# Optimization experiments

Measured on AMD Instinct MI355X. Metric: run time of the kernel, lower is better.

Reference implementation:

```python
import jax, jax.numpy as jnp
import numpy as np

N_EXPERTS = 64
TOPK = 4
DIM = 2048
B_T = 8192


def setup_inputs() -> dict:
    key = jax.random.key(0)
    k1, k2 = jax.random.split(key)
    x = jax.random.normal(k1, (B_T, DIM), jnp.float32)
    W = jax.random.normal(k2, (N_EXPERTS, DIM), jnp.float32) * 0.02  # nn.Linear weight (out, in)
    router_bias = jnp.zeros((N_EXPERTS,), jnp.float32)  # registered buffer, init zeros
    return {"x": x, "W": W, "router_bias": router_bias, "token_capacity": 3072}


def _route(x, W, router_bias, token_capacity):
    """Faithful serial greedy capacity-aware routing.

    Replicates the torch nested loop (k-major, token-minor order):
      - per step, pick argmax over the token's (mutated) logits among experts
        with remaining capacity;
      - full experts whose logit exceeds the chosen one get permanently set
        to -inf in that token's logit row (exactly what the inner while-style
        loop does);
      - if no expert has capacity, selected stays -1, weight 0, and the whole
        row becomes -inf (torch sets the top expert to -inf n_experts times).
    """
    logits0 = x @ W.T + router_bias                       # (N, E)
    scores = jax.nn.softmax(logits0, axis=-1)             # (N, E)
    cap = token_capacity // TOPK                          # python int
    remaining0 = jnp.full((N_EXPERTS,), float(cap), jnp.float32)
    N = x.shape[0]
    NEG = jnp.float32(-jnp.inf)

    def step(carry, i):
        logits, remaining = carry
        b = i % N                                         # token index (k-major order)
        row = logits[b]                                   # (E,)
        masked = jnp.where(remaining > 0, row, NEG)
        chosen = jnp.argmax(masked)
        ok = remaining[chosen] > 0                        # False only if all experts full
        sel = jnp.where(ok, chosen, -1).astype(jnp.int32)
        w = jnp.where(ok, scores[b, chosen], jnp.float32(0.0))
        full = remaining <= 0
        cval = row[chosen]
        # full experts 'above' the chosen one were visited and zapped to -inf
        new_row = jnp.where(ok,
                            jnp.where(full & (row > cval), NEG, row),
                            jnp.full_like(row, NEG))
        logits = logits.at[b].set(new_row)
        remaining = remaining.at[chosen].add(jnp.where(ok, jnp.float32(-1.0), jnp.float32(0.0)))
        return (logits, remaining), (sel, w)

    (_, _), (sel_f, w_f) = jax.lax.scan(step, (logits0, remaining0),
                                        jnp.arange(TOPK * N))
    selected = sel_f.reshape(TOPK, N).T                   # (N, TOPK)
    weights = w_f.reshape(TOPK, N).T                      # (N, TOPK)
    weights = weights / (weights.sum(axis=-1, keepdims=True) + 1e-8)
    return selected, weights


def reference(x, W, router_bias, token_capacity):
    return _route(x, W, router_bias, token_capacity)
```

## Files before the change

kernel.cpp:

```cpp
#include <hip/hip_runtime.h>
#include <math.h>

#define N_TOK 8192
#define DIM   2048
#define NE    64
#define TOPK  4
#define THETA 2e-3f
#define TPB   32
#define NBLK  (N_TOK / TPB)
#define HSTR  16

typedef short bf16x8 __attribute__((ext_vector_type(8)));
typedef float f32x4  __attribute__((ext_vector_type(4)));

#define OFF_LOGITS 0
#define OFF_MAXV   (OFF_LOGITS + N_TOK * NE)
#define OFF_DENOM  (OFF_MAXV + N_TOK)
#define OFF_HIST   (OFF_DENOM + N_TOK)
#define OFF_WH     (OFF_HIST + NE * HSTR)
#define OFF_WL     (OFF_WH + NE * DIM / 2)
#define OFF_WT     (OFF_WL + NE * DIM / 2)
#define OFF_WTMP   (OFF_WT + NE * DIM)

__device__ inline void cvt2(float a, float b, unsigned& hi, unsigned& lo) {
    const unsigned ua = __float_as_uint(a), ub = __float_as_uint(b);
    hi = __builtin_amdgcn_perm(ub, ua, 0x07060302u);
    const float ra = a - __uint_as_float(ua & 0xFFFF0000u);
    const float rb = b - __uint_as_float(ub & 0xFFFF0000u);
    lo = __builtin_amdgcn_perm(__float_as_uint(rb), __float_as_uint(ra), 0x07060302u);
}

union FragU { unsigned u[4]; bf16x8 v; uint4 q; };

__device__ inline void make_frags(const float4& p, const float4& q,
                                  bf16x8& hi, bf16x8& lo) {
    FragU H, L;
    cvt2(p.x, p.y, H.u[0], L.u[0]);
    cvt2(p.z, p.w, H.u[1], L.u[1]);
    cvt2(q.x, q.y, H.u[2], L.u[2]);
    cvt2(q.z, q.w, H.u[3], L.u[3]);
    hi = H.v; lo = L.v;
}

__global__ __launch_bounds__(256)
void k_wc(const float* __restrict__ W, unsigned short* __restrict__ wh2,
          unsigned short* __restrict__ wl2, float* __restrict__ wt,
          int* __restrict__ hist) {
    const int t = blockIdx.x * 256 + threadIdx.x;
    if (t < NE * HSTR) hist[t] = 0;
    const int l  = t & 63;
    const int grp = t >> 6;
    const int nt = grp & 3;
    const int kc = grp >> 2;
    const int e  = nt * 16 + (l & 15);
    const int k0 = kc * 32 + (l >> 4) * 8;

    const float4 p = *reinterpret_cast<const float4*>(W + (size_t)e * DIM + k0);
    const float4 q = *reinterpret_cast<const float4*>(W + (size_t)e * DIM + k0 + 4);
    FragU H, L;
    cvt2(p.x, p.y, H.u[0], L.u[0]);
    cvt2(p.z, p.w, H.u[1], L.u[1]);
    cvt2(q.x, q.y, H.u[2], L.u[2]);
    cvt2(q.z, q.w, H.u[3], L.u[3]);
    const size_t off = (size_t)grp * 512 + l * 8;
    *reinterpret_cast<uint4*>(wh2 + off) = H.q;
    *reinterpret_cast<uint4*>(wl2 + off) = L.q;

    wt[(size_t)(k0 + 0) * NE + e] = p.x;
    wt[(size_t)(k0 + 1) * NE + e] = p.y;
    wt[(size_t)(k0 + 2) * NE + e] = p.z;
    wt[(size_t)(k0 + 3) * NE + e] = p.w;
    wt[(size_t)(k0 + 4) * NE + e] = q.x;
    wt[(size_t)(k0 + 5) * NE + e] = q.y;
    wt[(size_t)(k0 + 6) * NE + e] = q.z;
    wt[(size_t)(k0 + 7) * NE + e] = q.w;
}

__global__ __launch_bounds__(512, 2)
void k_main(const float* __restrict__ x, const unsigned short* __restrict__ wh2,
            const unsigned short* __restrict__ wl2, const float* __restrict__ bias,
            const float* __restrict__ wt,
            float* __restrict__ logits, float* __restrict__ maxv,
            float* __restrict__ denomv, int* __restrict__ hist,
            float* __restrict__ out) {
    __shared__ __align__(16) char smem[98304];
    __shared__ float lbuf[TPB][68];
    __shared__ float part[8][68];
    __shared__ int   selS[TPB];
    __shared__ float wS[TPB];
    __shared__ short flagIdx[TPB];
    __shared__ int   flagCnt;

    const int tid = threadIdx.x;
    const int ww  = tid >> 6;
    const int l   = tid & 63;
    const int t0  = blockIdx.x * TPB;
    const int m   = l & 15;
    const int g   = l >> 4;
    const int tg  = ww >> 2;
    const int eg  = ww & 3;

    if (tid == 0) flagCnt = 0;

    auto stage = [&](int win) {
        #pragma unroll
        for (int j = 0; j < 12; ++j) {
            const int dbase = ww * 12288 + j * 1024;
            const int d = dbase + l * 16;
            const char* src;
            if (dbase < 32768) {
                const int r = d >> 10;
                const int s = ((d >> 4) & 63) ^ (r & 7);
                src = (const char*)(x + (size_t)(t0 + r) * DIM + win * 256 + s * 4);
            } else if (dbase < 65536) {
                src = (const char*)wh2 + (size_t)win * 32768 + (d - 32768);
            } else {
                src = (const char*)wl2 + (size_t)win * 32768 + (d - 65536);
            }
            __builtin_amdgcn_global_load_lds(
                (const __attribute__((address_space(1))) void*)src,
                (__attribute__((address_space(3))) void*)(smem + dbase),
                16, 0, 0);
        }
    };

    stage(0);
    asm volatile("s_waitcnt vmcnt(0)" ::: "memory");
    __syncthreads();

    f32x4 accA, accB;
    #pragma unroll
    for (int r = 0; r < 4; ++r) { accA[r] = 0.0f; accB[r] = 0.0f; }

    const int   arow  = tg * 16 + m;
    const char* aBase = smem + arow * 1024;
    const int   axor  = arow & 7;
    const char* bhB   = smem + 32768 + eg * 1024 + l * 16;

    for (int win = 0; win < 8; ++win) {
        #pragma unroll
        for (int kc = 0; kc < 8; ++kc) {
            const int s0 = kc * 8 + g * 2;
            const float4 p = *reinterpret_cast<const float4*>(aBase + ((s0 ^ axor) << 4));
            const float4 q = *reinterpret_cast<const float4*>(aBase + (((s0 + 1) ^ axor) << 4));
            FragU bh_, bl_;
            bh_.q = *reinterpret_cast<const uint4*>(bhB + kc * 4096);
            bl_.q = *reinterpret_cast<const uint4*>(bhB + 32768 + kc * 4096);
            bf16x8 ah, al;
            make_frags(p, q, ah, al);
            accA = __builtin_amdgcn_mfma_f32_16x16x32_bf16(ah, bh_.v, accA, 0, 0, 0);
            accB = __builtin_amdgcn_mfma_f32_16x16x32_bf16(al, bh_.v, accB, 0, 0, 0);
            accB = __builtin_amdgcn_mfma_f32_16x16x32_bf16(ah, bl_.v, accB, 0, 0, 0);
        }
        if (win < 7) {
            __syncthreads();
            stage(win + 1);
            asm volatile("s_waitcnt vmcnt(0)" ::: "memory");
            __syncthreads();
        }
    }

    {
        const float be = bias[eg * 16 + m];
        #pragma unroll
        for (int r = 0; r < 4; ++r)
            lbuf[tg * 16 + g * 4 + r][eg * 16 + m] = accA[r] + accB[r] + be;
    }
    __syncthreads();

    for (int e2 = tid; e2 < TPB * NE; e2 += 512) {
        const int t = e2 >> 6, e = e2 & 63;
        logits[(size_t)(t0 + t) * NE + e] = lbuf[t][e];
    }

    #pragma unroll
    for (int tt = 0; tt < 4; ++tt) {
        const int t = ww * 4 + tt;
        const float lv = lbuf[t][l];
        float v1 = lv; int i1 = l; float v2 = -INFINITY;
        #pragma unroll
        for (int off = 32; off; off >>= 1) {
            const float ov1 = __shfl_xor(v1, off);
            const int   oi1 = __shfl_xor(i1, off);
            const float ov2 = __shfl_xor(v2, off);
            if (ov1 > v1 || (ov1 == v1 && oi1 < i1)) {
                v2 = fmaxf(v1, ov2); v1 = ov1; i1 = oi1;
            } else {
                v2 = fmaxf(v2, ov1);
            }
        }
        float s = expf(lv - v1);
        #pragma unroll
        for (int off = 32; off; off >>= 1) s += __shfl_xor(s, off);
        if (l == 0) {
            const int row = t0 + t;
            maxv[row]   = v1;
            denomv[row] = s;
            selS[t]     = i1;
            wS[t]       = 1.0f / s;
            if (v1 - v2 < THETA) {
                const int ix = atomicAdd(&flagCnt, 1);
                flagIdx[ix] = (short)t;
            }
        }
    }
    __syncthreads();

    const int nf = flagCnt;
    for (int fi = 0; fi < nf; ++fi) {
        const int tl  = flagIdx[fi];
        const int row = t0 + tl;
        const float* xr = x + (size_t)row * DIM + ww * 256;
        const float* wb = wt + (size_t)(ww * 256) * NE + l;
        float a0 = 0.0f, a1 = 0.0f;
        #pragma unroll 4
        for (int k = 0; k < 256; k += 8) {
            const float4 x0 = *reinterpret_cast<const float4*>(xr + k);
            const float4 x1 = *reinterpret_cast<const float4*>(xr + k + 4);
            a0 = fmaf(x0.x, wb[(size_t)(k + 0) * NE], a0);
            a0 = fmaf(x0.y, wb[(size_t)(k + 1) * NE], a0);
            a0 = fmaf(x0.z, wb[(size_t)(k + 2) * NE], a0);
            a0 = fmaf(x0.w, wb[(size_t)(k + 3) * NE], a0);
            a1 = fmaf(x1.x, wb[(size_t)(k + 4) * NE], a1);
            a1 = fmaf(x1.y, wb[(size_t)(k + 5) * NE], a1);
            a1 = fmaf(x1.z, wb[(size_t)(k + 6) * NE], a1);
            a1 = fmaf(x1.w, wb[(size_t)(k + 7) * NE], a1);
        }
        part[ww][l] = a0 + a1;
        __syncthreads();
        if (ww == 0) {
            float lg = bias[l];
            #pragma unroll
            for (int s2 = 0; s2 < 8; ++s2) lg += part[s2][l];
            logits[(size_t)row * NE + l] = lg;
            float v = lg; int idx = l;
            #pragma unroll
            for (int off = 32; off; off >>= 1) {
                const float ov = __shfl_xor(v, off);
                const int   oi = __shfl_xor(idx, off);
                if (ov > v || (ov == v && oi < idx)) { v = ov; idx = oi; }
            }
            float p = expf(lg - v);
            #pragma unroll
            for (int off = 32; off; off >>= 1) p += __shfl_xor(p, off);
            if (l == 0) {
                maxv[row]   = v;
                denomv[row] = p;
                selS[tl]    = idx;
                wS[tl]      = 1.0f / p;
            }
        }
        __syncthreads();
    }

    if (ww == 0) {
        int cnt = 0;
        #pragma unroll
        for (int t = 0; t < TPB; ++t) cnt += (selS[t] == l) ? 1 : 0;
        if (cnt) atomicAdd(&hist[l * HSTR], cnt);
    }

    if (tid < TPB) {
        const int row = t0 + tid;
        const float se = (float)selS[tid];
        const float wv = wS[tid];
        const float wn = wv / (4.0f * wv + 1e-8f);
        *reinterpret_cast<float4*>(out + (size_t)row * 4) = make_float4(se, se, se, se);
        *reinterpret_cast<float4*>(out + (size_t)N_TOK * TOPK + (size_t)row * 4) =
            make_float4(wn, wn, wn, wn);
    }
}

__global__ __launch_bounds__(256)
void k_decide(const int* __restrict__ hist, const float* __restrict__ logits,
              const float* __restrict__ maxv, const float* __restrict__ denomv,
              const int* __restrict__ tc, float* __restrict__ out,
              float* __restrict__ wtmp) {
    __shared__ int flagS;
    const int tid = threadIdx.x;
    const int cap = tc[0] / TOPK;
    if (tid < NE) {
        const bool bad = (TOPK * hist[tid * HSTR] > cap);
        const unsigned long long mm = __ballot(bad);
        if (tid == 0) flagS = (mm == 0ull) ? 1 : 0;
    }
    __syncthreads();
    if (flagS) return;

    if (tid < 64) {
        const int e = tid;
        int rem = cap;
        for (int k = 0; k < TOPK; ++k) {
            for (int b = 0; b < N_TOK; ++b) {
                const float lg = logits[(size_t)b * NE + e];
                float v = (rem > 0) ? lg : -INFINITY;
                int idx = e;
                #pragma unroll
                for (int off = 32; off; off >>= 1) {
                    const float ov = __shfl_xor(v, off);
                    const int   oi = __shfl_xor(idx, off);
                    if (ov > v || (ov == v && oi < idx)) { v = ov; idx = oi; }
                }
                const bool ok = (v != -INFINITY);
                if (ok && e == idx) rem -= 1;
                const float lc = __shfl(lg, idx);
                if (e == 0) {
                    out[(size_t)b * TOPK + k]  = ok ? (float)idx : -1.0f;
                    wtmp[(size_t)b * TOPK + k] = ok ? expf(lc - maxv[b]) / denomv[b] : 0.0f;
                }
            }
        }
    }
    __syncthreads();
    for (int b = tid; b < N_TOK; b += 256) {
        const float w0 = wtmp[b * 4 + 0], w1_ = wtmp[b * 4 + 1];
        const float w2 = wtmp[b * 4 + 2], w3 = wtmp[b * 4 + 3];
        const float s = ((w0 + w1_) + w2) + w3 + 1e-8f;
        out[N_TOK * TOPK + b * 4 + 0] = w0 / s;
        out[N_TOK * TOPK + b * 4 + 1] = w1_ / s;
        out[N_TOK * TOPK + b * 4 + 2] = w2 / s;
        out[N_TOK * TOPK + b * 4 + 3] = w3 / s;
    }
}

extern "C" void kernel_launch(void* const* d_in, const int* in_sizes, int n_in,
                              void* d_out, int out_size, void* d_ws, size_t ws_size,
                              hipStream_t stream) {
    const float* x    = (const float*)d_in[0];
    const float* W    = (const float*)d_in[1];
    const float* bias = (const float*)d_in[2];
    const int*   tc   = (const int*)d_in[3];

    float* ws       = (float*)d_ws;
    float* logits   = ws + OFF_LOGITS;
    float* maxv     = ws + OFF_MAXV;
    float* denomv   = ws + OFF_DENOM;
    int*   hist     = (int*)(ws + OFF_HIST);
    unsigned short* wh2 = (unsigned short*)(ws + OFF_WH);
    unsigned short* wl2 = (unsigned short*)(ws + OFF_WL);
    float* wt       = ws + OFF_WT;
    float* wtmp     = ws + OFF_WTMP;
    float* out      = (float*)d_out;

    k_wc<<<NE * DIM / 8 / 256, 256, 0, stream>>>(W, wh2, wl2, wt, hist);
    k_main<<<NBLK, 512, 0, stream>>>(x, wh2, wl2, bias, wt, logits, maxv,
                                     denomv, hist, out);
    k_decide<<<1, 256, 0, stream>>>(hist, logits, maxv, denomv, tc, out, wtmp);
}
```

Measured before the change: 152.6 us.

## Double-buffer LDS staging and split K across waves with smem reduction

Splits the LDS tile into two half-size buffers and prefetches the next K-window while computing on the current one, removing the load-then-wait stall between windows. Waves now split the K dimension and each covers all 64 experts with four accumulator tiles, and the partial sums are reduced through shared memory before the bias add. Each window now has one barrier instead of two, but there are twice as many windows and the added reduction step costs extra LDS traffic and more accumulator registers.

```diff
diff --git a/kernel.cpp b/kernel.cpp
--- a/kernel.cpp
+++ b/kernel.cpp
@@ -83,7 +83,7 @@
             float* __restrict__ logits, float* __restrict__ maxv,
             float* __restrict__ denomv, int* __restrict__ hist,
             float* __restrict__ out) {
-    __shared__ __align__(16) char smem[98304];
+    __shared__ __align__(16) char smem[2][49152];
     __shared__ float lbuf[TPB][68];
     __shared__ float part[8][68];
     __shared__ int   selS[TPB];
@@ -98,80 +98,94 @@
     const int m   = l & 15;
     const int g   = l >> 4;
     const int tg  = ww >> 2;
-    const int eg  = ww & 3;
+    const int kcl = ww & 3;
 
     if (tid == 0) flagCnt = 0;
 
-    auto stage = [&](int win) {
-        #pragma unroll
-        for (int j = 0; j < 12; ++j) {
-            const int dbase = ww * 12288 + j * 1024;
+    auto stage = [&](int win, int bufsel) {
+        #pragma unroll
+        for (int j = 0; j < 6; ++j) {
+            const int dbase = ww * 6144 + j * 1024;
             const int d = dbase + l * 16;
             const char* src;
-            if (dbase < 32768) {
-                const int r = d >> 10;
-                const int s = ((d >> 4) & 63) ^ (r & 7);
-                src = (const char*)(x + (size_t)(t0 + r) * DIM + win * 256 + s * 4);
-            } else if (dbase < 65536) {
-                src = (const char*)wh2 + (size_t)win * 32768 + (d - 32768);
+            if (dbase < 16384) {
+                const int r = d >> 9;
+                const int p = (d >> 4) & 31;
+                const int s = p ^ (r & 15);
+                src = (const char*)(x + (size_t)(t0 + r) * DIM + win * 128 + s * 4);
+            } else if (dbase < 32768) {
+                src = (const char*)wh2 + (size_t)win * 16384 + (d - 16384);
             } else {
-                src = (const char*)wl2 + (size_t)win * 32768 + (d - 65536);
+                src = (const char*)wl2 + (size_t)win * 16384 + (d - 32768);
             }
             __builtin_amdgcn_global_load_lds(
                 (const __attribute__((address_space(1))) void*)src,
-                (__attribute__((address_space(3))) void*)(smem + dbase),
+                (__attribute__((address_space(3))) void*)(&smem[bufsel][dbase]),
                 16, 0, 0);
         }
     };
 
-    stage(0);
+    stage(0, 0);
     asm volatile("s_waitcnt vmcnt(0)" ::: "memory");
     __syncthreads();
 
-    f32x4 accA, accB;
+    f32x4 accA[4], accB[4];
     #pragma unroll
-    for (int r = 0; r < 4; ++r) { accA[r] = 0.0f; accB[r] = 0.0f; }
-
-    const int   arow  = tg * 16 + m;
-    const char* aBase = smem + arow * 1024;
-    const int   axor  = arow & 7;
-    const char* bhB   = smem + 32768 + eg * 1024 + l * 16;
-
-    for (int win = 0; win < 8; ++win) {
-        #pragma unroll
-        for (int kc = 0; kc < 8; ++kc) {
-            const int s0 = kc * 8 + g * 2;
-            const float4 p = *reinterpret_cast<const float4*>(aBase + ((s0 ^ axor) << 4));
-            const float4 q = *reinterpret_cast<const float4*>(aBase + (((s0 + 1) ^ axor) << 4));
-            FragU bh_, bl_;
-            bh_.q = *reinterpret_cast<const uint4*>(bhB + kc * 4096);
-            bl_.q = *reinterpret_cast<const uint4*>(bhB + 32768 + kc * 4096);
-            bf16x8 ah, al;
-            make_frags(p, q, ah, al);
-            accA = __builtin_amdgcn_mfma_f32_16x16x32_bf16(ah, bh_.v, accA, 0, 0, 0);
-            accB = __builtin_amdgcn_mfma_f32_16x16x32_bf16(al, bh_.v, accB, 0, 0, 0);
-            accB = __builtin_amdgcn_mfma_f32_16x16x32_bf16(ah, bl_.v, accB, 0, 0, 0);
-        }
-        if (win < 7) {
-            __syncthreads();
-            stage(win + 1);
-            asm volatile("s_waitcnt vmcnt(0)" ::: "memory");
-            __syncthreads();
-        }
-    }
-
-    {
-        const float be = bias[eg * 16 + m];
+    for (int nt = 0; nt < 4; ++nt)
+        #pragma unroll
+        for (int r = 0; r < 4; ++r) { accA[nt][r] = 0.0f; accB[nt][r] = 0.0f; }
+
+    const int arow = tg * 16 + m;
+    const int ax   = arow & 15;
+    const int s0   = kcl * 8 + g * 2;
+
+    for (int win = 0; win < 16; ++win) {
+        const int cur = win & 1;
+        if (win < 15) stage(win + 1, cur ^ 1);
+
+        const char* A  = smem[cur] + arow * 512;
+        const char* Bh = smem[cur] + 16384 + kcl * 4096 + l * 16;
+        const char* Bl = smem[cur] + 32768 + kcl * 4096 + l * 16;
+
+        const float4 p = *reinterpret_cast<const float4*>(A + ((s0 ^ ax) << 4));
+        const float4 q = *reinterpret_cast<const float4*>(A + (((s0 + 1) ^ ax) << 4));
+        bf16x8 ah, al;
+        make_frags(p, q, ah, al);
+
+        #pragma unroll
+        for (int nt = 0; nt < 4; ++nt) {
+            FragU b; b.q = *reinterpret_cast<const uint4*>(Bh + nt * 1024);
+            accA[nt] = __builtin_amdgcn_mfma_f32_16x16x32_bf16(ah, b.v, accA[nt], 0, 0, 0);
+            accB[nt] = __builtin_amdgcn_mfma_f32_16x16x32_bf16(al, b.v, accB[nt], 0, 0, 0);
+        }
+        #pragma unroll
+        for (int nt = 0; nt < 4; ++nt) {
+            FragU b; b.q = *reinterpret_cast<const uint4*>(Bl + nt * 1024);
+            accB[nt] = __builtin_amdgcn_mfma_f32_16x16x32_bf16(ah, b.v, accB[nt], 0, 0, 0);
+        }
+
+        asm volatile("s_waitcnt vmcnt(0)" ::: "memory");
+        __syncthreads();
+    }
+
+    float* red = reinterpret_cast<float*>(&smem[0][0]);
+    #pragma unroll
+    for (int nt = 0; nt < 4; ++nt)
         #pragma unroll
         for (int r = 0; r < 4; ++r)
-            lbuf[tg * 16 + g * 4 + r][eg * 16 + m] = accA[r] + accB[r] + be;
-    }
+            red[(kcl * TPB + tg * 16 + g * 4 + r) * 68 + nt * 16 + m] =
+                accA[nt][r] + accB[nt][r];
     __syncthreads();
 
     for (int e2 = tid; e2 < TPB * NE; e2 += 512) {
         const int t = e2 >> 6, e = e2 & 63;
-        logits[(size_t)(t0 + t) * NE + e] = lbuf[t][e];
-    }
+        float s = red[(0 * TPB + t) * 68 + e] + red[(1 * TPB + t) * 68 + e]
+                + red[(2 * TPB + t) * 68 + e] + red[(3 * TPB + t) * 68 + e];
+        s += bias[e];
+        logits[(size_t)(t0 + t) * NE + e] = s;
+        lbuf[t][e] = s;
+    }
+    __syncthreads();
 
     #pragma unroll
     for (int tt = 0; tt < 4; ++tt) {
```

Result: no change. 149.6 us (-1.9%).

## Split K across two blocks per token strip with last-arriver reduction

Applied to the files above, without the earlier changes.

Doubles the grid so each 32-token strip runs as two blocks, each covering half of the 2048-wide reduction. Each block writes its partial logits to workspace, and an atomic arrival counter picks the second finisher to sum the partials, add bias and run the routing epilogue. Shared memory is halved and launch bounds move to 4 blocks per CU, aiming to fill more of the 256 CUs and raise occupancy on a grid of only 256 blocks. The cost is extra global traffic for the partials, thread fences and the atomic, and the first finisher's epilogue work is simply skipped.

```diff
diff --git a/kernel.cpp b/kernel.cpp
--- a/kernel.cpp
+++ b/kernel.cpp
@@ -7,17 +7,20 @@
 #define TOPK  4
 #define THETA 2e-3f
 #define TPB   32
-#define NBLK  (N_TOK / TPB)
+#define NSTRIP (N_TOK / TPB)
+#define NBLK2 (NSTRIP * 2)
 #define HSTR  16
 
 typedef short bf16x8 __attribute__((ext_vector_type(8)));
 typedef float f32x4  __attribute__((ext_vector_type(4)));
 
 #define OFF_LOGITS 0
-#define OFF_MAXV   (OFF_LOGITS + N_TOK * NE)
+#define OFF_P1     (OFF_LOGITS + N_TOK * NE)
+#define OFF_MAXV   (OFF_P1 + N_TOK * NE)
 #define OFF_DENOM  (OFF_MAXV + N_TOK)
 #define OFF_HIST   (OFF_DENOM + N_TOK)
-#define OFF_WH     (OFF_HIST + NE * HSTR)
+#define OFF_CNT    (OFF_HIST + NE * HSTR)
+#define OFF_WH     (OFF_CNT + 320)
 #define OFF_WL     (OFF_WH + NE * DIM / 2)
 #define OFF_WT     (OFF_WL + NE * DIM / 2)
 #define OFF_WTMP   (OFF_WT + NE * DIM)
@@ -45,9 +48,10 @@
 __global__ __launch_bounds__(256)
 void k_wc(const float* __restrict__ W, unsigned short* __restrict__ wh2,
           unsigned short* __restrict__ wl2, float* __restrict__ wt,
-          int* __restrict__ hist) {
+          int* __restrict__ hist, int* __restrict__ cnt) {
     const int t = blockIdx.x * 256 + threadIdx.x;
     if (t < NE * HSTR) hist[t] = 0;
+    if (t < 320) cnt[t] = 0;
     const int l  = t & 63;
     const int grp = t >> 6;
     const int nt = grp & 3;
@@ -76,107 +80,110 @@
     wt[(size_t)(k0 + 7) * NE + e] = q.w;
 }
 
-__global__ __launch_bounds__(512, 2)
+__global__ __launch_bounds__(512, 4)
 void k_main(const float* __restrict__ x, const unsigned short* __restrict__ wh2,
             const unsigned short* __restrict__ wl2, const float* __restrict__ bias,
-            const float* __restrict__ wt,
-            float* __restrict__ logits, float* __restrict__ maxv,
+            const float* __restrict__ wt, float* __restrict__ p0,
+            float* __restrict__ p1, float* __restrict__ maxv,
             float* __restrict__ denomv, int* __restrict__ hist,
-            float* __restrict__ out) {
-    __shared__ __align__(16) char smem[98304];
-    __shared__ float lbuf[TPB][68];
-    __shared__ float part[8][68];
-    __shared__ int   selS[TPB];
-    __shared__ float wS[TPB];
-    __shared__ short flagIdx[TPB];
-    __shared__ int   flagCnt;
-
-    const int tid = threadIdx.x;
-    const int ww  = tid >> 6;
-    const int l   = tid & 63;
-    const int t0  = blockIdx.x * TPB;
-    const int m   = l & 15;
-    const int g   = l >> 4;
-    const int tg  = ww >> 2;
-    const int eg  = ww & 3;
-
-    if (tid == 0) flagCnt = 0;
-
-    auto stage = [&](int win) {
-        #pragma unroll
-        for (int j = 0; j < 12; ++j) {
-            const int dbase = ww * 12288 + j * 1024;
+            int* __restrict__ cnt, float* __restrict__ out) {
+    __shared__ __align__(16) char smem[49152];
+    __shared__ int flagCnt, arrive;
+
+    const int tid   = threadIdx.x;
+    const int ww    = tid >> 6;
+    const int l     = tid & 63;
+    const int strip = blockIdx.x >> 1;
+    const int khalf = blockIdx.x & 1;
+    const int t0    = strip * TPB;
+    const int m     = l & 15;
+    const int g     = l >> 4;
+    const int tg    = ww >> 2;
+    const int eg    = ww & 3;
+
+    f32x4 accA, accB;
+    #pragma unroll
+    for (int r = 0; r < 4; ++r) { accA[r] = 0.0f; accB[r] = 0.0f; }
+
+    const int arow = tg * 16 + m;
+    const int axor = arow & 15;
+
+    for (int win = 0; win < 8; ++win) {
+        #pragma unroll
+        for (int j = 0; j < 6; ++j) {
+            const int dbase = ww * 6144 + j * 1024;
             const int d = dbase + l * 16;
             const char* src;
-            if (dbase < 32768) {
-                const int r = d >> 10;
-                const int s = ((d >> 4) & 63) ^ (r & 7);
-                src = (const char*)(x + (size_t)(t0 + r) * DIM + win * 256 + s * 4);
-            } else if (dbase < 65536) {
-                src = (const char*)wh2 + (size_t)win * 32768 + (d - 32768);
+            if (dbase < 16384) {
+                const int r = d >> 9;
+                const int p = (d >> 4) & 31;
+                const int s = p ^ (r & 15);
+                src = (const char*)(x + (size_t)(t0 + r) * DIM
+                                    + khalf * 1024 + win * 128 + s * 4);
+            } else if (dbase < 32768) {
+                src = (const char*)wh2 + (size_t)(khalf * 8 + win) * 16384 + (d - 16384);
             } else {
-                src = (const char*)wl2 + (size_t)win * 32768 + (d - 65536);
+                src = (const char*)wl2 + (size_t)(khalf * 8 + win) * 16384 + (d - 32768);
             }
             __builtin_amdgcn_global_load_lds(
                 (const __attribute__((address_space(1))) void*)src,
                 (__attribute__((address_space(3))) void*)(smem + dbase),
                 16, 0, 0);
         }
-    };
-
-    stage(0);
-    asm volatile("s_waitcnt vmcnt(0)" ::: "memory");
-    __syncthreads();
-
-    f32x4 accA, accB;
-    #pragma unroll
-    for (int r = 0; r < 4; ++r) { accA[r] = 0.0f; accB[r] = 0.0f; }
-
-    const int   arow  = tg * 16 + m;
-    const char* aBase = smem + arow * 1024;
-    const int   axor  = arow & 7;
-    const char* bhB   = smem + 32768 + eg * 1024 + l * 16;
-
-    for (int win = 0; win < 8; ++win) {
-        #pragma unroll
-        for (int kc = 0; kc < 8; ++kc) {
+        asm volatile("s_waitcnt vmcnt(0)" ::: "memory");
+        __syncthreads();
+
+        const char* A = smem + arow * 512;
+        #pragma unroll
+        for (int kc = 0; kc < 4; ++kc) {
             const int s0 = kc * 8 + g * 2;
-            const float4 p = *reinterpret_cast<const float4*>(aBase + ((s0 ^ axor) << 4));
-            const float4 q = *reinterpret_cast<const float4*>(aBase + (((s0 + 1) ^ axor) << 4));
+            const float4 pf = *reinterpret_cast<const float4*>(A + ((s0 ^ axor) << 4));
+            const float4 qf = *reinterpret_cast<const float4*>(A + (((s0 + 1) ^ axor) << 4));
+            bf16x8 ah, al;
+            make_frags(pf, qf, ah, al);
             FragU bh_, bl_;
-            bh_.q = *reinterpret_cast<const uint4*>(bhB + kc * 4096);
-            bl_.q = *reinterpret_cast<const uint4*>(bhB + 32768 + kc * 4096);
-            bf16x8 ah, al;
-            make_frags(p, q, ah, al);
+            bh_.q = *reinterpret_cast<const uint4*>(smem + 16384 + (kc * 4 + eg) * 1024 + l * 16);
+            bl_.q = *reinterpret_cast<const uint4*>(smem + 32768 + (kc * 4 + eg) * 1024 + l * 16);
             accA = __builtin_amdgcn_mfma_f32_16x16x32_bf16(ah, bh_.v, accA, 0, 0, 0);
             accB = __builtin_amdgcn_mfma_f32_16x16x32_bf16(al, bh_.v, accB, 0, 0, 0);
             accB = __builtin_amdgcn_mfma_f32_16x16x32_bf16(ah, bl_.v, accB, 0, 0, 0);
         }
-        if (win < 7) {
-            __syncthreads();
-            stage(win + 1);
-            asm volatile("s_waitcnt vmcnt(0)" ::: "memory");
-            __syncthreads();
-        }
+        __syncthreads();
     }
 
     {
-        const float be = bias[eg * 16 + m];
+        float* dst = khalf ? p1 : p0;
         #pragma unroll
         for (int r = 0; r < 4; ++r)
-            lbuf[tg * 16 + g * 4 + r][eg * 16 + m] = accA[r] + accB[r] + be;
-    }
-    __syncthreads();
-
+            dst[(size_t)(t0 + tg * 16 + g * 4 + r) * NE + eg * 16 + m] = accA[r] + accB[r];
+    }
+    __threadfence();
+    __syncthreads();
+    if (tid == 0) arrive = atomicAdd(&cnt[strip], 1);
+    __syncthreads();
+    if (arrive == 0) return;
+    __threadfence();
+
+    float* lbuf    = reinterpret_cast<float*>(smem);
+    float* part    = reinterpret_cast<float*>(smem + 8704);
+    int*   selS    = reinterpret_cast<int*>(smem + 10880);
+    float* wS      = reinterpret_cast<float*>(smem + 11008);
+    short* flagIdx = reinterpret_cast<short*>(smem + 11136);
+
+    if (tid == 0) flagCnt = 0;
     for (int e2 = tid; e2 < TPB * NE; e2 += 512) {
         const int t = e2 >> 6, e = e2 & 63;
-        logits[(size_t)(t0 + t) * NE + e] = lbuf[t][e];
-    }
+        const size_t idx = (size_t)(t0 + t) * NE + e;
+        const float s = p0[idx] + p1[idx] + bias[e];
+        p0[idx] = s;
+        lbuf[t * 68 + e] = s;
+    }
+    __syncthreads();
 
     #pragma unroll
     for (int tt = 0; tt < 4; ++tt) {
         const int t = ww * 4 + tt;
-        const float lv = lbuf[t][l];
+        const float lv = lbuf[t * 68 + l];
         float v1 = lv; int i1 = l; float v2 = -INFINITY;
         #pragma unroll
         for (int off = 32; off; off >>= 1) {
@@ -226,13 +233,13 @@
             a1 = fmaf(x1.z, wb[(size_t)(k + 6) * NE], a1);
             a1 = fmaf(x1.w, wb[(size_t)(k + 7) * NE], a1);
         }
-        part[ww][l] = a0 + a1;
+        part[ww * 68 + l] = a0 + a1;
         __syncthreads();
         if (ww == 0) {
             float lg = bias[l];
             #pragma unroll
-            for (int s2 = 0; s2 < 8; ++s2) lg += part[s2][l];
-            logits[(size_t)row * NE + l] = lg;
+            for (int s2 = 0; s2 < 8; ++s2) lg += part[s2 * 68 + l];
+            p0[(size_t)row * NE + l] = lg;
             float v = lg; int idx = l;
             #pragma unroll
             for (int off = 32; off; off >>= 1) {
@@ -254,10 +261,10 @@
     }
 
     if (ww == 0) {
-        int cnt = 0;
-        #pragma unroll
-        for (int t = 0; t < TPB; ++t) cnt += (selS[t] == l) ? 1 : 0;
-        if (cnt) atomicAdd(&hist[l * HSTR], cnt);
+        int cnt2 = 0;
+        #pragma unroll
+        for (int t = 0; t < TPB; ++t) cnt2 += (selS[t] == l) ? 1 : 0;
+        if (cnt2) atomicAdd(&hist[l * HSTR], cnt2);
     }
 
     if (tid < TPB) {
@@ -333,17 +340,19 @@
 
     float* ws       = (float*)d_ws;
     float* logits   = ws + OFF_LOGITS;
+    float* p1       = ws + OFF_P1;
     float* maxv     = ws + OFF_MAXV;
     float* denomv   = ws + OFF_DENOM;
     int*   hist     = (int*)(ws + OFF_HIST);
+    int*   cnt      = (int*)(ws + OFF_CNT);
     unsigned short* wh2 = (unsigned short*)(ws + OFF_WH);
     unsigned short* wl2 = (unsigned short*)(ws + OFF_WL);
     float* wt       = ws + OFF_WT;
     float* wtmp     = ws + OFF_WTMP;
     float* out      = (float*)d_out;
 
-    k_wc<<<NE * DIM / 8 / 256, 256, 0, stream>>>(W, wh2, wl2, wt, hist);
-    k_main<<<NBLK, 512, 0, stream>>>(x, wh2, wl2, bias, wt, logits, maxv,
-                                     denomv, hist, out);
+    k_wc<<<NE * DIM / 8 / 256, 256, 0, stream>>>(W, wh2, wl2, wt, hist, cnt);
+    k_main<<<NBLK2, 512, 0, stream>>>(x, wh2, wl2, bias, wt, logits, p1,
+                                      maxv, denomv, hist, cnt, out);
     k_decide<<<1, 256, 0, stream>>>(hist, logits, maxv, denomv, tc, out, wtmp);
 }
```

Result: slower. 322.4 us (+111.3%).
